# Kernel tuning notes

Hardware: AMD Instinct MI355X
Metric: run time of the kernel (lower is better)

The kernel has to match this reference:

```python
import jax, jax.numpy as jnp
import numpy as np

H = 20      # LSTM hidden size (hard-coded in module)
FF = 64     # linear1 out
B = 131072  # batch
T = 256     # input_length


def _init_lstm(key, in_dim, hid):
    k1, k2, k3, k4 = jax.random.split(key, 4)
    s = 1.0 / np.sqrt(hid)
    return (
        jax.random.uniform(k1, (4 * hid, in_dim), jnp.float32, -s, s),
        jax.random.uniform(k2, (4 * hid, hid), jnp.float32, -s, s),
        jax.random.uniform(k3, (4 * hid,), jnp.float32, -s, s),
        jax.random.uniform(k4, (4 * hid,), jnp.float32, -s, s),
    )


def setup_inputs() -> dict:
    key = jax.random.key(0)
    ks = jax.random.split(key, 7)
    diagnosis = jax.random.normal(ks[0], (B, T), jnp.float32)
    W_ih1, W_hh1, b_ih1, b_hh1 = _init_lstm(ks[1], 1, H)
    W_ih2, W_hh2, b_ih2, b_hh2 = _init_lstm(ks[2], H, H)
    s1 = 1.0 / np.sqrt(H)
    W1 = jax.random.uniform(ks[3], (FF, H), jnp.float32, -s1, s1)
    b1 = jax.random.uniform(ks[4], (FF,), jnp.float32, -s1, s1)
    s2 = 1.0 / np.sqrt(FF)
    W2 = jax.random.uniform(ks[5], (1, FF), jnp.float32, -s2, s2)
    b2 = jax.random.uniform(ks[6], (1,), jnp.float32, -s2, s2)
    return {"diagnosis": diagnosis,
            "W_ih1": W_ih1, "W_hh1": W_hh1, "b_ih1": b_ih1, "b_hh1": b_hh1,
            "W_ih2": W_ih2, "W_hh2": W_hh2, "b_ih2": b_ih2, "b_hh2": b_hh2,
            "W1": W1, "b1": b1, "W2": W2, "b2": b2}


def _lstm_cell(x, h, c, W_ih, W_hh, b_ih, b_hh):
    # PyTorch LSTMCell gate ordering: i, f, g, o
    z = x @ W_ih.T + h @ W_hh.T + b_ih + b_hh  # [B, 4H]
    i, f, g, o = jnp.split(z, 4, axis=-1)
    c_new = jax.nn.sigmoid(f) * c + jax.nn.sigmoid(i) * jnp.tanh(g)
    h_new = jax.nn.sigmoid(o) * jnp.tanh(c_new)
    return h_new, c_new


def reference(diagnosis, W_ih1, W_hh1, b_ih1, b_hh1,
              W_ih2, W_hh2, b_ih2, b_hh2, W1, b1, W2, b2):
    bsz = diagnosis.shape[0]
    xs = diagnosis.T[:, :, None]  # [T, B, 1]
    zeros = jnp.zeros((bsz, H), diagnosis.dtype)

    def step(carry, x_t):
        h1, c1, h2, c2 = carry
        h1, c1 = _lstm_cell(x_t, h1, c1, W_ih1, W_hh1, b_ih1, b_hh1)
        h2, c2 = _lstm_cell(h1, h2, c2, W_ih2, W_hh2, b_ih2, b_hh2)
        return (h1, c1, h2, c2), None

    (h1, c1, h2, c2), _ = jax.lax.scan(step, (zeros, zeros, zeros, zeros), xs)
    y1 = jax.nn.relu(h2 @ W1.T + b1)
    y2 = jax.nn.relu(y1 @ W2.T + b2)  # [B, 1]
    return y2
```

## Files before the change

kernel.cpp:

```cpp
#include <hip/hip_runtime.h>

#define HH 20
#define TSTEPS 256
#define FF 64
#define EPW 32
#define NB 2
#define ROWLEN 72
#define LOG2E 1.44269504088896f

typedef __attribute__((ext_vector_type(8))) _Float16 f16x8;
typedef __attribute__((ext_vector_type(2))) _Float16 f16x2;
typedef __attribute__((ext_vector_type(4))) float    f32x4;
typedef __attribute__((ext_vector_type(2))) float    f32x2;

__device__ __forceinline__ f32x4 mfma16(f16x8 a, f16x8 b, f32x4 c) {
    return __builtin_amdgcn_mfma_f32_16x16x32_f16(a, b, c, 0, 0, 0);
}
__device__ __forceinline__ float rcpf(float x) { return __builtin_amdgcn_rcpf(x); }
__device__ __forceinline__ float exp2fast(float x) {
#if __has_builtin(__builtin_amdgcn_exp2f)
    return __builtin_amdgcn_exp2f(x);
#else
    return __expf(x * 0.6931471805599453f);
#endif
}

__device__ __forceinline__ f32x2 act_pair(f32x4 za, f32x4 zb, f32x2& c) {
    f32x2 ei; ei.x = exp2fast(za.x); ei.y = exp2fast(zb.x);
    f32x2 ef; ef.x = exp2fast(za.y); ef.y = exp2fast(zb.y);
    f32x2 eg; eg.x = exp2fast(za.z); eg.y = exp2fast(zb.z);
    f32x2 eo; eo.x = exp2fast(za.w); eo.y = exp2fast(zb.w);
    const f32x2 one = {1.0f, 1.0f};
    f32x2 P = (one + ei) * (one + eg);
    f32x2 Q = one + ef;
    f32x2 num = c * P + (eg - one) * Q;
    f32x2 den = P * Q;
    f32x2 r; r.x = rcpf(den.x); r.y = rcpf(den.y);
    c = num * r;
    f32x2 sc = c * (2.0f * LOG2E);
    sc.x = fminf(sc.x, 100.0f); sc.y = fminf(sc.y, 100.0f);
    f32x2 ec; ec.x = exp2fast(sc.x); ec.y = exp2fast(sc.y);
    f32x2 den2 = (one + eo) * (one + ec);
    f32x2 r2; r2.x = rcpf(den2.x); r2.y = rcpf(den2.y);
    return (ec - one) * r2;
}
__device__ __forceinline__ float act_one(f32x4 za, float& c) {
    float ei = exp2fast(za.x), ef = exp2fast(za.y);
    float eg = exp2fast(za.z), eo = exp2fast(za.w);
    float P = (1.0f + ei) * (1.0f + eg);
    float Q = 1.0f + ef;
    float num = fmaf(c, P, (eg - 1.0f) * Q);
    c = num * rcpf(P * Q);
    float sc = fminf(c * (2.0f * LOG2E), 100.0f);
    float ec = exp2fast(sc);
    float r2 = rcpf((1.0f + eo) * (1.0f + ec));
    return (ec - 1.0f) * r2;
}

__global__ void prep_weights(
    const float* __restrict__ Wih1, const float* __restrict__ Whh1,
    const float* __restrict__ bih1, const float* __restrict__ bhh1,
    const float* __restrict__ Wih2, const float* __restrict__ Whh2,
    const float* __restrict__ bih2, const float* __restrict__ bhh2,
    _Float16* __restrict__ ws)
{
    const int t0 = blockIdx.x * blockDim.x + threadIdx.x;
    const int stride = blockDim.x * gridDim.x;
    for (int idx = t0; idx < 80 * 32; idx += stride) {
        int r = idx >> 5, k = idx & 31;
        int m = r >> 4, q = (r >> 2) & 3, g = r & 3;
        int u = 5 * q + m, ro = g * HH + u;
        float s = (g == 2) ? 2.0f * LOG2E : -LOG2E;
        float v = 0.0f;
        if (k < 24)       { int qc = k / 6, wc = k % 6; if (wc < 5) v = Whh1[ro * HH + 5 * qc + wc]; }
        else if (k == 24)   v = Wih1[ro];
        else if (k == 25)   v = bih1[ro] + bhh1[ro];
        ws[idx] = (_Float16)(s * v);
    }
    for (int idx = t0; idx < 80 * 64; idx += stride) {
        int r = idx >> 6, k = idx & 63;
        int m = r >> 4, q = (r >> 2) & 3, g = r & 3;
        int u = 5 * q + m, ro = g * HH + u;
        float s = (g == 2) ? 2.0f * LOG2E : -LOG2E;
        float v = 0.0f;
        if (k < 24)       { int qc = k / 6, wc = k % 6; if (wc < 5) v = Wih2[ro * HH + 5 * qc + wc]; }
        else if (k == 25)   v = bih2[ro] + bhh2[ro];
        else if (k >= 26 && k < 50) {
            int cH = k - 26, qc = cH / 6, wc = cH % 6;
            if (wc < 5) v = Whh2[ro * HH + 5 * qc + wc];
        }
        ws[2560 + idx] = (_Float16)(s * v);
    }
}

__global__ __launch_bounds__(64, 4) void lstm_mfma(
    const float* __restrict__ diag,
    const _Float16* __restrict__ wpk,
    const float* __restrict__ W1, const float* __restrict__ b1,
    const float* __restrict__ W2, const float* __restrict__ b2,
    float* __restrict__ out, int Btot)
{
    __shared__ _Float16 s_B[EPW * ROWLEN];

    const int lane = threadIdx.x;
    const int q  = lane >> 4;
    const int cc = lane & 15;
    const int e  = blockIdx.x * EPW + (lane & (EPW - 1));
    const int esafe = (e < Btot) ? e : (Btot - 1);

    if (lane < EPW) {
        uint4 zz = {0u, 0u, 0u, 0u};
        #pragma unroll
        for (int j = 0; j < 9; ++j)
            *(uint4*)((char*)s_B + lane * 144 + j * 16) = zz;
    }

    f16x8 A1[5], A2a[5], A2b[5];
    {
        const _Float16* W2c = wpk + 2560;
        const int kb = q * 8;
        #pragma unroll
        for (int m = 0; m < 5; ++m) {
            const int r = 16 * m + cc;
            A1[m]  = *(const f16x8*)(wpk + r * 32 + kb);
            A2a[m] = *(const f16x8*)(W2c + r * 64 + kb);
            A2b[m] = *(const f16x8*)(W2c + r * 64 + 32 + kb);
        }
    }

    f32x2 c1p[NB][2], c2p[NB][2];
    float c1s[NB], c2s[NB];
    #pragma unroll
    for (int n = 0; n < NB; ++n) {
        c1p[n][0] = (f32x2){0.0f, 0.0f}; c1p[n][1] = (f32x2){0.0f, 0.0f};
        c2p[n][0] = (f32x2){0.0f, 0.0f}; c2p[n][1] = (f32x2){0.0f, 0.0f};
        c1s[n] = 0.0f; c2s[n] = 0.0f;
    }

    const float* __restrict__ xr = diag + (long long)esafe * TSTEPS;
    float x = xr[0];
    const f32x4 zz4 = {0.0f, 0.0f, 0.0f, 0.0f};

    #pragma unroll 1
    for (int t = 0; t < TSTEPS; ++t) {
        float xn = xr[(t + 1) & (TSTEPS - 1)];

        if (lane < EPW) {
            f16x2 pk; pk.x = (_Float16)x; pk.y = (_Float16)1.0f;
            *(f16x2*)(s_B + lane * ROWLEN + 24) = pk;
        }

        #pragma unroll
        for (int n = 0; n < NB; ++n) {
            const _Float16* rowp = s_B + (n * 16 + cc) * ROWLEN;
            f16x8 bf = *(const f16x8*)(rowp + 8 * q);
            f32x4 z0 = mfma16(A1[0], bf, zz4);
            f32x4 z1 = mfma16(A1[1], bf, zz4);
            f32x4 z2 = mfma16(A1[2], bf, zz4);
            f32x4 z3 = mfma16(A1[3], bf, zz4);
            f32x4 z4 = mfma16(A1[4], bf, zz4);
            _Float16* wp = s_B + (n * 16 + cc) * ROWLEN + 6 * q;
            f32x2 h01 = act_pair(z0, z1, c1p[n][0]);
            { f16x2 o; o.x = (_Float16)h01.x; o.y = (_Float16)h01.y; *(f16x2*)(wp) = o; }
            f32x2 h23 = act_pair(z2, z3, c1p[n][1]);
            { f16x2 o; o.x = (_Float16)h23.x; o.y = (_Float16)h23.y; *(f16x2*)(wp + 2) = o; }
            float h4 = act_one(z4, c1s[n]);
            wp[4] = (_Float16)h4;
        }

        #pragma unroll
        for (int n = 0; n < NB; ++n) {
            const _Float16* rowp = s_B + (n * 16 + cc) * ROWLEN;
            f16x8 b0  = *(const f16x8*)(rowp + 8 * q);
            f16x8 b1f = *(const f16x8*)(rowp + 32 + 8 * q);
            f32x4 z0 = mfma16(A2b[0], b1f, mfma16(A2a[0], b0, zz4));
            f32x4 z1 = mfma16(A2b[1], b1f, mfma16(A2a[1], b0, zz4));
            f32x4 z2 = mfma16(A2b[2], b1f, mfma16(A2a[2], b0, zz4));
            f32x4 z3 = mfma16(A2b[3], b1f, mfma16(A2a[3], b0, zz4));
            f32x4 z4 = mfma16(A2b[4], b1f, mfma16(A2a[4], b0, zz4));
            _Float16* wp = s_B + (n * 16 + cc) * ROWLEN + 26 + 6 * q;
            f32x2 h01 = act_pair(z0, z1, c2p[n][0]);
            { f16x2 o; o.x = (_Float16)h01.x; o.y = (_Float16)h01.y; *(f16x2*)(wp) = o; }
            f32x2 h23 = act_pair(z2, z3, c2p[n][1]);
            { f16x2 o; o.x = (_Float16)h23.x; o.y = (_Float16)h23.y; *(f16x2*)(wp + 2) = o; }
            float h4 = act_one(z4, c2s[n]);
            wp[4] = (_Float16)h4;
        }

        x = xn;
    }

    if (lane < EPW && e < Btot) {
        const _Float16* rowp = s_B + lane * ROWLEN + 26;
        float hv[HH];
        #pragma unroll
        for (int qq = 0; qq < 4; ++qq)
            #pragma unroll
            for (int ww = 0; ww < 5; ++ww)
                hv[5 * qq + ww] = (float)rowp[6 * qq + ww];

        float y2 = b2[0];
        #pragma unroll 1
        for (int jj = 0; jj < FF; ++jj) {
            float a = b1[jj];
            const float* __restrict__ wj = W1 + jj * HH;
            #pragma unroll
            for (int k = 0; k < HH; ++k)
                a = fmaf(hv[k], wj[k], a);
            a = fmaxf(a, 0.0f);
            y2 = fmaf(a, W2[jj], y2);
        }
        out[e] = fmaxf(y2, 0.0f);
    }
}

extern "C" void kernel_launch(void* const* d_in, const int* in_sizes, int n_in,
                              void* d_out, int out_size, void* d_ws, size_t ws_size,
                              hipStream_t stream)
{
    (void)n_in; (void)ws_size; (void)out_size;
    const float* diag = (const float*)d_in[0];
    const float* Wih1 = (const float*)d_in[1];
    const float* Whh1 = (const float*)d_in[2];
    const float* bih1 = (const float*)d_in[3];
    const float* bhh1 = (const float*)d_in[4];
    const float* Wih2 = (const float*)d_in[5];
    const float* Whh2 = (const float*)d_in[6];
    const float* bih2 = (const float*)d_in[7];
    const float* bhh2 = (const float*)d_in[8];
    const float* W1   = (const float*)d_in[9];
    const float* b1   = (const float*)d_in[10];
    const float* W2   = (const float*)d_in[11];
    const float* b2   = (const float*)d_in[12];

    const int Btot = in_sizes[0] / TSTEPS;
    _Float16* wpk = (_Float16*)d_ws;

    prep_weights<<<8, 256, 0, stream>>>(Wih1, Whh1, bih1, bhh1,
                                        Wih2, Whh2, bih2, bhh2, wpk);

    lstm_mfma<<<(Btot + EPW - 1) / EPW, 64, 0, stream>>>(
        diag, wpk, W1, b1, W2, b2, (float*)d_out, Btot);
}
```

Measured before the change: 1.277 ms.

## Offload sigmoid exp2 to FMA polynomial and use packed RTZ half conversion

```diff
diff --git a/kernel.cpp b/kernel.cpp
--- a/kernel.cpp
+++ b/kernel.cpp
@@ -13,23 +13,36 @@
 typedef __attribute__((ext_vector_type(4))) float    f32x4;
 typedef __attribute__((ext_vector_type(2))) float    f32x2;
 
+__device__ __forceinline__ f16x2 pkrtz(float a, float b) {
+    return __builtin_bit_cast(f16x2, __builtin_amdgcn_cvt_pkrtz(a, b));
+}
+
 __device__ __forceinline__ f32x4 mfma16(f16x8 a, f16x8 b, f32x4 c) {
     return __builtin_amdgcn_mfma_f32_16x16x32_f16(a, b, c, 0, 0, 0);
 }
 __device__ __forceinline__ float rcpf(float x) { return __builtin_amdgcn_rcpf(x); }
-__device__ __forceinline__ float exp2fast(float x) {
+__device__ __forceinline__ float exp2t(float x) {
 #if __has_builtin(__builtin_amdgcn_exp2f)
     return __builtin_amdgcn_exp2f(x);
 #else
     return __expf(x * 0.6931471805599453f);
 #endif
 }
+__device__ __forceinline__ float exp2v(float x) {
+    float n = __builtin_rintf(x);
+    float f = x - n;
+    float p = fmaf(f, 0.00961813f, 0.05550411f);
+    p = fmaf(f, p, 0.24022651f);
+    p = fmaf(f, p, 0.69314718f);
+    p = fmaf(f, p, 1.0f);
+    return __builtin_ldexpf(p, (int)n);
+}
 
 __device__ __forceinline__ f32x2 act_pair(f32x4 za, f32x4 zb, f32x2& c) {
-    f32x2 ei; ei.x = exp2fast(za.x); ei.y = exp2fast(zb.x);
-    f32x2 ef; ef.x = exp2fast(za.y); ef.y = exp2fast(zb.y);
-    f32x2 eg; eg.x = exp2fast(za.z); eg.y = exp2fast(zb.z);
-    f32x2 eo; eo.x = exp2fast(za.w); eo.y = exp2fast(zb.w);
+    f32x2 ei; ei.x = exp2v(za.x); ei.y = exp2v(zb.x);
+    f32x2 ef; ef.x = exp2v(za.y); ef.y = exp2v(zb.y);
+    f32x2 eg; eg.x = exp2t(za.z); eg.y = exp2t(zb.z);
+    f32x2 eo; eo.x = exp2v(za.w); eo.y = exp2v(zb.w);
     const f32x2 one = {1.0f, 1.0f};
     f32x2 P = (one + ei) * (one + eg);
     f32x2 Q = one + ef;
@@ -39,20 +52,20 @@
     c = num * r;
     f32x2 sc = c * (2.0f * LOG2E);
     sc.x = fminf(sc.x, 100.0f); sc.y = fminf(sc.y, 100.0f);
-    f32x2 ec; ec.x = exp2fast(sc.x); ec.y = exp2fast(sc.y);
+    f32x2 ec; ec.x = exp2t(sc.x); ec.y = exp2t(sc.y);
     f32x2 den2 = (one + eo) * (one + ec);
     f32x2 r2; r2.x = rcpf(den2.x); r2.y = rcpf(den2.y);
     return (ec - one) * r2;
 }
 __device__ __forceinline__ float act_one(f32x4 za, float& c) {
-    float ei = exp2fast(za.x), ef = exp2fast(za.y);
-    float eg = exp2fast(za.z), eo = exp2fast(za.w);
+    float ei = exp2v(za.x), ef = exp2v(za.y);
+    float eg = exp2t(za.z), eo = exp2v(za.w);
     float P = (1.0f + ei) * (1.0f + eg);
     float Q = 1.0f + ef;
     float num = fmaf(c, P, (eg - 1.0f) * Q);
     c = num * rcpf(P * Q);
     float sc = fminf(c * (2.0f * LOG2E), 100.0f);
-    float ec = exp2fast(sc);
+    float ec = exp2t(sc);
     float r2 = rcpf((1.0f + eo) * (1.0f + ec));
     return (ec - 1.0f) * r2;
 }
@@ -113,6 +126,7 @@
         #pragma unroll
         for (int j = 0; j < 9; ++j)
             *(uint4*)((char*)s_B + lane * 144 + j * 16) = zz;
+        s_B[lane * ROWLEN + 25] = (_Float16)1.0f;
     }
 
     f16x8 A1[5], A2a[5], A2b[5];
@@ -145,10 +159,8 @@
     for (int t = 0; t < TSTEPS; ++t) {
         float xn = xr[(t + 1) & (TSTEPS - 1)];
 
-        if (lane < EPW) {
-            f16x2 pk; pk.x = (_Float16)x; pk.y = (_Float16)1.0f;
-            *(f16x2*)(s_B + lane * ROWLEN + 24) = pk;
-        }
+        if (lane < EPW)
+            s_B[lane * ROWLEN + 24] = (_Float16)x;
 
         #pragma unroll
         for (int n = 0; n < NB; ++n) {
@@ -161,9 +173,9 @@
             f32x4 z4 = mfma16(A1[4], bf, zz4);
             _Float16* wp = s_B + (n * 16 + cc) * ROWLEN + 6 * q;
             f32x2 h01 = act_pair(z0, z1, c1p[n][0]);
-            { f16x2 o; o.x = (_Float16)h01.x; o.y = (_Float16)h01.y; *(f16x2*)(wp) = o; }
+            *(f16x2*)(wp) = pkrtz(h01.x, h01.y);
             f32x2 h23 = act_pair(z2, z3, c1p[n][1]);
-            { f16x2 o; o.x = (_Float16)h23.x; o.y = (_Float16)h23.y; *(f16x2*)(wp + 2) = o; }
+            *(f16x2*)(wp + 2) = pkrtz(h23.x, h23.y);
             float h4 = act_one(z4, c1s[n]);
             wp[4] = (_Float16)h4;
         }
@@ -180,9 +192,9 @@
             f32x4 z4 = mfma16(A2b[4], b1f, mfma16(A2a[4], b0, zz4));
             _Float16* wp = s_B + (n * 16 + cc) * ROWLEN + 26 + 6 * q;
             f32x2 h01 = act_pair(z0, z1, c2p[n][0]);
-            { f16x2 o; o.x = (_Float16)h01.x; o.y = (_Float16)h01.y; *(f16x2*)(wp) = o; }
+            *(f16x2*)(wp) = pkrtz(h01.x, h01.y);
             f32x2 h23 = act_pair(z2, z3, c2p[n][1]);
-            { f16x2 o; o.x = (_Float16)h23.x; o.y = (_Float16)h23.y; *(f16x2*)(wp + 2) = o; }
+            *(f16x2*)(wp + 2) = pkrtz(h23.x, h23.y);
             float h4 = act_one(z4, c2s[n]);
             wp[4] = (_Float16)h4;
         }
```

Result: slower. 1.774 ms (+38.9%).
